# Kernel tuning notes

Hardware: AMD Instinct MI355X
Metric: run time of the kernel (lower is better)

Reference implementation:

```python
import jax, jax.numpy as jnp
import numpy as np

N, E, G = 50000, 800000, 512
D_NODE, D_EDGE, D_HID, D_OUT = 64, 16, 64, 1


def _lin(key, din, dout, bias=True):
    k1, k2 = jax.random.split(key)
    w = jax.random.normal(k1, (din, dout), jnp.float32) / np.sqrt(din)
    if bias:
        b = jax.random.normal(k2, (dout,), jnp.float32) * 0.01
        return w, b
    return w


def setup_inputs() -> dict:
    key = jax.random.key(0)
    ks = jax.random.split(key, 24)
    x = jax.random.normal(ks[0], (N, D_NODE), jnp.float32)
    edge_index = jax.random.randint(ks[1], (2, E), 0, N, jnp.int64)
    edge_attr = jax.random.normal(ks[2], (E, D_EDGE), jnp.float32)
    batch = jnp.sort(jax.random.randint(ks[3], (N,), 0, G, jnp.int64))
    wq1, bq1 = _lin(ks[4], D_NODE, D_HID)
    wk1, bk1 = _lin(ks[5], D_NODE, D_HID)
    wv1, bv1 = _lin(ks[6], D_NODE, D_HID)
    we1 = _lin(ks[7], D_EDGE, D_HID, bias=False)
    ws1, bs1 = _lin(ks[8], D_NODE, D_HID)
    wq2, bq2 = _lin(ks[9], D_HID, D_HID)
    wk2, bk2 = _lin(ks[10], D_HID, D_HID)
    wv2, bv2 = _lin(ks[11], D_HID, D_HID)
    we2 = _lin(ks[12], D_EDGE, D_HID, bias=False)
    ws2, bs2 = _lin(ks[13], D_HID, D_HID)
    w_fc1, b_fc1 = _lin(ks[14], D_HID, D_HID)
    w_fc2, b_fc2 = _lin(ks[15], D_HID, D_OUT)
    return dict(x=x, edge_index=edge_index, edge_attr=edge_attr, batch=batch,
                wq1=wq1, bq1=bq1, wk1=wk1, bk1=bk1, wv1=wv1, bv1=bv1, we1=we1, ws1=ws1, bs1=bs1,
                wq2=wq2, bq2=bq2, wk2=wk2, bk2=bk2, wv2=wv2, bv2=bv2, we2=we2, ws2=ws2, bs2=bs2,
                w_fc1=w_fc1, b_fc1=b_fc1, w_fc2=w_fc2, b_fc2=b_fc2)


def _leaky(z):
    return jnp.where(z >= 0, z, 0.01 * z)


def _transformer_conv(x, src, dst, e, wq, bq, wk, bk, wv, bv, we, ws, bs):
    # PyG TransformerConv, heads=1, concat=True, root_weight=True
    C = wq.shape[1]
    q = x @ wq + bq                      # [N,C]
    k = x @ wk + bk                      # [N,C]
    v = x @ wv + bv                      # [N,C]
    ee = e @ we                          # [E,C] (lin_edge, bias=False)
    ke = k[src] + ee                     # per-edge key
    ve = v[src] + ee                     # per-edge value
    score = jnp.sum(q[dst] * ke, axis=-1) / jnp.sqrt(jnp.float32(C))  # [E]
    m = jax.ops.segment_max(score, dst, num_segments=N)
    a = jnp.exp(score - m[dst])
    den = jax.ops.segment_sum(a, dst, num_segments=N)
    den = jnp.where(den == 0, 1.0, den)
    alpha = a / den[dst]
    agg = jax.ops.segment_sum(alpha[:, None] * ve, dst, num_segments=N)
    return agg + x @ ws + bs             # skip connection


def reference(x, edge_index, edge_attr, batch,
              wq1, bq1, wk1, bk1, wv1, bv1, we1, ws1, bs1,
              wq2, bq2, wk2, bk2, wv2, bv2, we2, ws2, bs2,
              w_fc1, b_fc1, w_fc2, b_fc2):
    src, dst = edge_index[0], edge_index[1]
    h = _leaky(_transformer_conv(x, src, dst, edge_attr, wq1, bq1, wk1, bk1, wv1, bv1, we1, ws1, bs1))
    atom_embs = _leaky(_transformer_conv(h, src, dst, edge_attr, wq2, bq2, wk2, bk2, wv2, bv2, we2, ws2, bs2))
    pooled = jax.ops.segment_sum(atom_embs, batch, num_segments=G)    # [G,C]
    norm = jnp.linalg.norm(pooled, axis=1, keepdims=True)
    h = pooled / jnp.maximum(norm, 1e-12)                             # F.normalize p=2
    h = _leaky(h @ w_fc1 + b_fc1)
    out = h @ w_fc2 + b_fc2
    return (out, atom_embs)
```

## Files before the change

kernel.cpp:

```cpp
#include <hip/hip_runtime.h>
#include <hip/hip_bf16.h>
#include <math.h>


typedef unsigned int uint32;
typedef unsigned short u16;

__device__ __forceinline__ uint32 f2bf(float x) {
    uint32 u = __float_as_uint(x);
    u += 0x7fffu + ((u >> 16) & 1u);
    return u >> 16;
}
__device__ __forceinline__ float bf2f(u16 h) {
    return __uint_as_float(((uint32)h) << 16);
}


__global__ void hist_kernel(const int* __restrict__ dst, int* __restrict__ deg, int E) {
    int e = blockIdx.x * blockDim.x + threadIdx.x;
    if (e < E) atomicAdd(&deg[dst[e]], 1);
}

__global__ void scan1_kernel(const int* __restrict__ deg, int* __restrict__ row_ptr,
                             int* __restrict__ totals, int N) {
    __shared__ int sh[1024];
    int tid = threadIdx.x;
    int i = blockIdx.x * 1024 + tid;
    int d = (i < N) ? deg[i] : 0;
    int val = d;
    sh[tid] = val;
    __syncthreads();
    for (int off = 1; off < 1024; off <<= 1) {
        int add = (tid >= off) ? sh[tid - off] : 0;
        __syncthreads();
        val += add;
        sh[tid] = val;
        __syncthreads();
    }
    if (i < N) row_ptr[i] = val - d;
    if (tid == 1023) totals[blockIdx.x] = val;
}

__global__ void scan2_kernel(int* totals, int nb) {
    int lane = threadIdx.x;
    int v = (lane < nb) ? totals[lane] : 0;
    #pragma unroll
    for (int off = 1; off < 64; off <<= 1) {
        int t = __shfl_up(v, off);
        if (lane >= off) v += t;
    }
    int ex = __shfl_up(v, 1);
    if (lane == 0) ex = 0;
    if (lane < nb) totals[lane] = ex;
}

__global__ void scan3_kernel(int* __restrict__ row_ptr, const int* __restrict__ totals,
                             int N, int E) {
    int i = blockIdx.x * blockDim.x + threadIdx.x;
    if (i < N) row_ptr[i] += totals[i >> 10];
    if (i == 0) row_ptr[N] = E;
}

__global__ void scatter_kernel(const int* __restrict__ dst, const int* __restrict__ row_ptr,
                               int* __restrict__ fill, int* __restrict__ csr_eid, int E) {
    int e = blockIdx.x * blockDim.x + threadIdx.x;
    if (e < E) {
        int d = dst[e];
        int pos = row_ptr[d] + atomicAdd(&fill[d], 1);
        csr_eid[pos] = e;
    }
}

__global__ void convert_kernel(const int* __restrict__ csr_eid, const int* __restrict__ src,
                               const float* __restrict__ ea,
                               int* __restrict__ csr_src, u16* __restrict__ ea16, int E) {
    int p = blockIdx.x * blockDim.x + threadIdx.x;
    if (p >= E) return;
    int e = csr_eid[p];
    csr_src[p] = src[e];
    const float4* ev = (const float4*)(ea + (size_t)e * 16);
    float4 q0 = ev[0], q1 = ev[1], q2 = ev[2], q3 = ev[3];
    uint32* o = (uint32*)(ea16 + (size_t)p * 16);
    o[0] = f2bf(q0.x) | (f2bf(q0.y) << 16);
    o[1] = f2bf(q0.z) | (f2bf(q0.w) << 16);
    o[2] = f2bf(q1.x) | (f2bf(q1.y) << 16);
    o[3] = f2bf(q1.z) | (f2bf(q1.w) << 16);
    o[4] = f2bf(q2.x) | (f2bf(q2.y) << 16);
    o[5] = f2bf(q2.z) | (f2bf(q2.w) << 16);
    o[6] = f2bf(q3.x) | (f2bf(q3.y) << 16);
    o[7] = f2bf(q3.z) | (f2bf(q3.w) << 16);
}


__global__ void wqe_kernel(const float* __restrict__ wq1, const float* __restrict__ bq1,
                           const float* __restrict__ we1,
                           const float* __restrict__ wq2, const float* __restrict__ bq2,
                           const float* __restrict__ we2,
                           float* __restrict__ A1, float* __restrict__ be1,
                           float* __restrict__ A2, float* __restrict__ be2) {
    const float* wq = blockIdx.x ? wq2 : wq1;
    const float* bq = blockIdx.x ? bq2 : bq1;
    const float* we = blockIdx.x ? we2 : we1;
    float* A  = blockIdx.x ? A2 : A1;
    float* be = blockIdx.x ? be2 : be1;
    int t = threadIdx.x;
    for (int idx = t; idx < 64 * 16; idx += 256) {
        int dd = idx >> 4, j = idx & 15;
        float acc = 0.f;
        for (int c = 0; c < 64; ++c) acc = fmaf(wq[dd * 64 + c], we[j * 64 + c], acc);
        A[idx] = acc * 0.125f;
    }
    if (t < 16) {
        float acc = 0.f;
        for (int c = 0; c < 64; ++c) acc = fmaf(bq[c], we[t * 64 + c], acc);
        be[t] = acc * 0.125f;
    }
}


__global__ __launch_bounds__(256) void qkvs_kernel(
    const float* __restrict__ xin,
    const float* __restrict__ wqm, const float* __restrict__ bqm,
    const float* __restrict__ wkm, const float* __restrict__ bkm,
    const float* __restrict__ wvm, const float* __restrict__ bvm,
    const float* __restrict__ wsm, const float* __restrict__ bsm,
    const float* __restrict__ Aq, const float* __restrict__ beq,
    float* __restrict__ qo, uint32* __restrict__ kvo,
    float* __restrict__ so, float* __restrict__ qeo, int N)
{
    int mtx = blockIdx.y;
    __shared__ float W0[64][64];
    __shared__ float W1[64][64];
    __shared__ float X[64][64];
    __shared__ float As[64][17];
    int t = threadIdx.x;
    int col = t & 63;
    int sub = t >> 6;

    const float* w0 = (mtx == 0) ? wqm : (mtx == 1) ? wkm : wsm;
    const float* b0p = (mtx == 0) ? bqm : (mtx == 1) ? bkm : bsm;
    for (int r = t; r < 1024; r += 256) ((float4*)W0)[r] = ((const float4*)w0)[r];
    if (mtx == 1)
        for (int r = t; r < 1024; r += 256) ((float4*)W1)[r] = ((const float4*)wvm)[r];
    if (mtx == 0)
        for (int r = t; r < 1024; r += 256) As[r >> 4][r & 15] = Aq[r];
    int n0 = blockIdx.x * 64;
    if (n0 + 64 <= N) {
        const float4* xi4 = (const float4*)(xin + (size_t)n0 * 64);
        for (int r = t; r < 1024; r += 256) ((float4*)X)[r] = xi4[r];
    } else {
        for (int r = t; r < 4096; r += 256) {
            int n = n0 + (r >> 6);
            X[r >> 6][r & 63] = (n < N) ? xin[(size_t)n * 64 + (r & 63)] : 0.f;
        }
    }
    __syncthreads();

    float b0 = b0p[col];
    float b1 = (mtx == 1) ? bvm[col] : 0.f;

    for (int nb = sub * 16; nb < sub * 16 + 16; nb += 8) {
        float a0[8], a1[8];
        #pragma unroll
        for (int u = 0; u < 8; ++u) { a0[u] = b0; a1[u] = b1; }
        if (mtx == 1) {
            for (int j = 0; j < 64; ++j) {
                float wk_ = W0[j][col], wv_ = W1[j][col];
                #pragma unroll
                for (int u = 0; u < 8; ++u) {
                    float xv = X[nb + u][j];
                    a0[u] = fmaf(xv, wk_, a0[u]);
                    a1[u] = fmaf(xv, wv_, a1[u]);
                }
            }
        } else {
            for (int j = 0; j < 64; ++j) {
                float wj = W0[j][col];
                #pragma unroll
                for (int u = 0; u < 8; ++u) a0[u] = fmaf(X[nb + u][j], wj, a0[u]);
            }
        }
        #pragma unroll
        for (int u = 0; u < 8; ++u) {
            int n = n0 + nb + u;
            if (n < N) {
                if (mtx == 0)      qo[(size_t)n * 64 + col] = a0[u] * 0.125f;
                else if (mtx == 2) so[(size_t)n * 64 + col] = a0[u];
                else kvo[(size_t)n * 64 + col] = f2bf(a0[u]) | (f2bf(a1[u]) << 16);
            }
        }
    }

    if (mtx == 0) {
        #pragma unroll
        for (int rep = 0; rep < 4; ++rep) {
            int idx = rep * 256 + t;
            int n = idx >> 4, j = idx & 15;
            float acc = beq[j];
            for (int c = 0; c < 64; ++c) acc = fmaf(X[n][c], As[c][j], acc);
            int gn = n0 + n;
            if (gn < N) qeo[(size_t)gn * 16 + j] = acc;
        }
    }
}


__global__ __launch_bounds__(256) void agg_kernel(
    const float* __restrict__ q, const uint32* __restrict__ kv,
    const float* __restrict__ qe, const float* __restrict__ we,
    const u16* __restrict__ ea16,
    const int* __restrict__ row_ptr, const int* __restrict__ csr_src,
    const float* __restrict__ skip_in, float* __restrict__ hout,
    const int* __restrict__ batch, float* __restrict__ pooled, int N)
{
    int lane = threadIdx.x & 63;
    int wid = (blockIdx.x << 2) + (threadIdx.x >> 6);
    if (wid >= N) return;
    int i = __builtin_amdgcn_readfirstlane(wid);

    int grp = lane >> 4;
    int pos = lane & 15;

    float4 qv = ((const float4*)(q + (size_t)i * 64))[pos];
    float qel = qe[(size_t)i * 16 + pos];
    float wer[16];
    #pragma unroll
    for (int j = 0; j < 16; ++j) wer[j] = we[j * 64 + lane];

    float den = 0.f, aj = 0.f;
    float o4x = 0.f, o4y = 0.f, o4z = 0.f, o4w = 0.f;

    int beg = row_ptr[i], end = row_ptr[i + 1];
    int last = end - 1;
    for (int p = beg; p < end; p += 8) {
        int egA = p + grp, egB = p + 4 + grp;
        int siA = (egA < end) ? egA : last;
        int siB = (egB < end) ? egB : last;
        int sA = csr_src[siA], sB = csr_src[siB];
        uint4 kbA = ((const uint4*)(kv + (size_t)sA * 64))[pos];
        uint4 kbB = ((const uint4*)(kv + (size_t)sB * 64))[pos];
        float eaA = bf2f(ea16[(size_t)p * 16 + lane]);
        float eaB = bf2f(ea16[(size_t)(p + 4) * 16 + lane]);

        float pa = eaA * qel, pb = eaB * qel;
        pa = fmaf(qv.x, __uint_as_float(kbA.x << 16), pa);
        pb = fmaf(qv.x, __uint_as_float(kbB.x << 16), pb);
        pa = fmaf(qv.y, __uint_as_float(kbA.y << 16), pa);
        pb = fmaf(qv.y, __uint_as_float(kbB.y << 16), pb);
        pa = fmaf(qv.z, __uint_as_float(kbA.z << 16), pa);
        pb = fmaf(qv.z, __uint_as_float(kbB.z << 16), pb);
        pa = fmaf(qv.w, __uint_as_float(kbA.w << 16), pa);
        pb = fmaf(qv.w, __uint_as_float(kbB.w << 16), pb);
        pa += __shfl_xor(pa, 1);  pb += __shfl_xor(pb, 1);
        pa += __shfl_xor(pa, 2);  pb += __shfl_xor(pb, 2);
        pa += __shfl_xor(pa, 4);  pb += __shfl_xor(pb, 4);
        pa += __shfl_xor(pa, 8);  pb += __shfl_xor(pb, 8);
        float scA = (egA < end) ? pa : -1e30f;
        float scB = (egB < end) ? pb : -1e30f;
        float wA = __expf(scA), wB = __expf(scB);

        den += wA + wB;
        aj = fmaf(wA, eaA, aj);
        aj = fmaf(wB, eaB, aj);
        o4x = fmaf(wA, __uint_as_float(kbA.x & 0xffff0000u), o4x);
        o4y = fmaf(wA, __uint_as_float(kbA.y & 0xffff0000u), o4y);
        o4z = fmaf(wA, __uint_as_float(kbA.z & 0xffff0000u), o4z);
        o4w = fmaf(wA, __uint_as_float(kbA.w & 0xffff0000u), o4w);
        o4x = fmaf(wB, __uint_as_float(kbB.x & 0xffff0000u), o4x);
        o4y = fmaf(wB, __uint_as_float(kbB.y & 0xffff0000u), o4y);
        o4z = fmaf(wB, __uint_as_float(kbB.z & 0xffff0000u), o4z);
        o4w = fmaf(wB, __uint_as_float(kbB.w & 0xffff0000u), o4w);
    }

    o4x += __shfl_xor(o4x, 16); o4x += __shfl_xor(o4x, 32);
    o4y += __shfl_xor(o4y, 16); o4y += __shfl_xor(o4y, 32);
    o4z += __shfl_xor(o4z, 16); o4z += __shfl_xor(o4z, 32);
    o4w += __shfl_xor(o4w, 16); o4w += __shfl_xor(o4w, 32);
    aj  += __shfl_xor(aj, 16);  aj  += __shfl_xor(aj, 32);
    den += __shfl_xor(den, 16); den += __shfl_xor(den, 32);

    int srcl = lane >> 2;
    float t0 = __shfl(o4x, srcl), t1 = __shfl(o4y, srcl);
    float t2 = __shfl(o4z, srcl), t3 = __shfl(o4w, srcl);
    int r2 = lane & 3;
    float o = (r2 == 0) ? t0 : (r2 == 1) ? t1 : (r2 == 2) ? t2 : t3;

    #pragma unroll
    for (int j = 0; j < 16; ++j) o = fmaf(__shfl(aj, j), wer[j], o);

    float dinv = (den > 0.f) ? 1.f / den : 0.f;
    float r = fmaf(o, dinv, skip_in[(size_t)i * 64 + lane]);
    r = (r >= 0.f) ? r : 0.01f * r;
    hout[(size_t)i * 64 + lane] = r;
    if (pooled) atomicAdd(&pooled[(size_t)batch[i] * 64 + lane], r);
}


__global__ void head_kernel(const float* __restrict__ pooled,
                            const float* __restrict__ w1, const float* __restrict__ b1,
                            const float* __restrict__ w2, const float* __restrict__ b2,
                            float* __restrict__ out, int G) {
    int g = blockIdx.x;
    int lane = threadIdx.x;
    __shared__ float hl[64];
    float p = pooled[g * 64 + lane];
    float ss = p * p;
    #pragma unroll
    for (int off = 32; off; off >>= 1) ss += __shfl_xor(ss, off);
    float hn = p / fmaxf(sqrtf(ss), 1e-12f);
    hl[lane] = hn;
    __syncthreads();
    float acc = b1[lane];
    #pragma unroll
    for (int j = 0; j < 64; ++j) acc = fmaf(hl[j], w1[j * 64 + lane], acc);
    acc = (acc >= 0.f) ? acc : 0.01f * acc;
    float r = acc * w2[lane];
    #pragma unroll
    for (int off = 32; off; off >>= 1) r += __shfl_xor(r, off);
    if (lane == 0) out[g] = r + b2[0];
}


extern "C" void kernel_launch(void* const* d_in, const int* in_sizes, int n_in,
                              void* d_out, int out_size, void* d_ws, size_t ws_size,
                              hipStream_t stream) {
    const float* x     = (const float*)d_in[0];
    const int*   ei    = (const int*)  d_in[1];
    const float* ea    = (const float*)d_in[2];
    const int*   batch = (const int*)  d_in[3];
    const float *wq1=(const float*)d_in[4],  *bq1=(const float*)d_in[5];
    const float *wk1=(const float*)d_in[6],  *bk1=(const float*)d_in[7];
    const float *wv1=(const float*)d_in[8],  *bv1=(const float*)d_in[9];
    const float *we1=(const float*)d_in[10];
    const float *ws1=(const float*)d_in[11], *bs1=(const float*)d_in[12];
    const float *wq2=(const float*)d_in[13], *bq2=(const float*)d_in[14];
    const float *wk2=(const float*)d_in[15], *bk2=(const float*)d_in[16];
    const float *wv2=(const float*)d_in[17], *bv2=(const float*)d_in[18];
    const float *we2=(const float*)d_in[19];
    const float *ws2=(const float*)d_in[20], *bs2=(const float*)d_in[21];
    const float *wf1=(const float*)d_in[22], *bf1=(const float*)d_in[23];
    const float *wf2=(const float*)d_in[24], *bf2=(const float*)d_in[25];

    int N = in_sizes[0] / 64;
    int E = in_sizes[2] / 16;
    int G = out_size - N * 64;

    const int* srcA = ei;
    const int* dstA = ei + E;

    char* w = (char*)d_ws;
    float*  qb      = (float*)w;  w += (size_t)N * 64 * 4;
    uint32* kvb     = (uint32*)w; w += (size_t)N * 64 * 4;
    float*  hb      = (float*)w;  w += (size_t)N * 64 * 4;
    float*  qeb     = (float*)w;  w += (size_t)N * 16 * 4;
    float*  pooled  = (float*)w;  w += (size_t)G * 64 * 4;
    int* row_ptr    = (int*)w;    w += (size_t)(N + 1) * 4;
    int* totals     = (int*)w;    w += 256 * 4;
    float* A1       = (float*)w;  w += 1024 * 4;
    float* be1      = (float*)w;  w += 16 * 4;
    float* A2       = (float*)w;  w += 1024 * 4;
    float* be2      = (float*)w;  w += 16 * 4;
    int* csr_src    = (int*)w;    w += (size_t)E * 4;
    int* csr_eid    = (int*)w;    w += (size_t)E * 4;
    u16* ea16       = (u16*)w;    w += (size_t)(E * 16 + 128) * 2;
    int* deg  = (int*)qb;
    int* fill = (int*)qb + N;

    hipMemsetAsync(deg, 0, (size_t)2 * N * 4, stream);
    hipMemsetAsync(pooled, 0, (size_t)G * 64 * 4, stream);

    const int TB = 256;
    wqe_kernel<<<2, 256, 0, stream>>>(wq1, bq1, we1, wq2, bq2, we2, A1, be1, A2, be2);
    hist_kernel<<<(E + TB - 1) / TB, TB, 0, stream>>>(dstA, deg, E);
    int nb = (N + 1023) / 1024;
    scan1_kernel<<<nb, 1024, 0, stream>>>(deg, row_ptr, totals, N);
    scan2_kernel<<<1, 64, 0, stream>>>(totals, nb);
    scan3_kernel<<<(N + TB - 1) / TB, TB, 0, stream>>>(row_ptr, totals, N, E);
    scatter_kernel<<<(E + TB - 1) / TB, TB, 0, stream>>>(dstA, row_ptr, fill, csr_eid, E);
    convert_kernel<<<(E + TB - 1) / TB, TB, 0, stream>>>(csr_eid, srcA, ea,
                                                         csr_src, ea16, E);

    float* outp = (float*)d_out;
    float* atom = outp + G;

    dim3 qgrid((N + 63) / 64, 3);
    int aggBlocks = (N + 3) / 4;

    qkvs_kernel<<<qgrid, 256, 0, stream>>>(x, wq1, bq1, wk1, bk1, wv1, bv1, ws1, bs1,
                                           A1, be1, qb, kvb, hb, qeb, N);
    agg_kernel<<<aggBlocks, 256, 0, stream>>>(qb, kvb, qeb, we1, ea16, row_ptr, csr_src,
                                              hb, hb, nullptr, nullptr, N);

    qkvs_kernel<<<qgrid, 256, 0, stream>>>(hb, wq2, bq2, wk2, bk2, wv2, bv2, ws2, bs2,
                                           A2, be2, qb, kvb, atom, qeb, N);
    agg_kernel<<<aggBlocks, 256, 0, stream>>>(qb, kvb, qeb, we2, ea16, row_ptr, csr_src,
                                              atom, atom, batch, pooled, N);

    head_kernel<<<G, 64, 0, stream>>>(pooled, wf1, bf1, wf2, bf2, outp, G);
}
```

Baseline: 449.4 us.

## Compute node projections with bf16 MFMA and pre-transposed packed weights

Replaces the scalar FP32 shared-memory GEMM for the Q/K/V/skip and Q·We projections with bf16 MFMA 16x16x32 instructions. A prep kernel transposes and packs all layer weights to bf16, including the folded query-edge matrix. One launch per layer now computes every projection, where the old version used three grid slices that each reloaded X. This lowers FP32 ALU work and redundant input reads, but rounds inputs and weights to bf16, which reduces the precision of q, skip and qe.

```diff
diff --git a/kernel.cpp b/kernel.cpp
--- a/kernel.cpp
+++ b/kernel.cpp
@@ -5,6 +5,8 @@
 
 typedef unsigned int uint32;
 typedef unsigned short u16;
+typedef __attribute__((ext_vector_type(8))) short short8;
+typedef __attribute__((ext_vector_type(4))) float f32x4;
 
 __device__ __forceinline__ uint32 f2bf(float x) {
     uint32 u = __float_as_uint(x);
@@ -92,23 +94,38 @@
 }
 
 
-__global__ void wqe_kernel(const float* __restrict__ wq1, const float* __restrict__ bq1,
-                           const float* __restrict__ we1,
-                           const float* __restrict__ wq2, const float* __restrict__ bq2,
-                           const float* __restrict__ we2,
-                           float* __restrict__ A1, float* __restrict__ be1,
-                           float* __restrict__ A2, float* __restrict__ be2) {
-    const float* wq = blockIdx.x ? wq2 : wq1;
-    const float* bq = blockIdx.x ? bq2 : bq1;
-    const float* we = blockIdx.x ? we2 : we1;
-    float* A  = blockIdx.x ? A2 : A1;
-    float* be = blockIdx.x ? be2 : be1;
+__global__ void wprep_kernel(
+    const float* __restrict__ wq1, const float* __restrict__ bq1,
+    const float* __restrict__ wk1, const float* __restrict__ wv1,
+    const float* __restrict__ ws1, const float* __restrict__ we1,
+    const float* __restrict__ wq2, const float* __restrict__ bq2,
+    const float* __restrict__ wk2, const float* __restrict__ wv2,
+    const float* __restrict__ ws2, const float* __restrict__ we2,
+    u16* __restrict__ wt1, float* __restrict__ be1,
+    u16* __restrict__ wt2, float* __restrict__ be2)
+{
+    int L = blockIdx.x;
+    const float* wq = L ? wq2 : wq1;
+    const float* bq = L ? bq2 : bq1;
+    const float* wk = L ? wk2 : wk1;
+    const float* wv = L ? wv2 : wv1;
+    const float* ws = L ? ws2 : ws1;
+    const float* we = L ? we2 : we1;
+    u16* wt = L ? wt2 : wt1;
+    float* be = L ? be2 : be1;
     int t = threadIdx.x;
-    for (int idx = t; idx < 64 * 16; idx += 256) {
-        int dd = idx >> 4, j = idx & 15;
+    for (int i = t; i < 4096; i += 256) {
+        int k = i >> 6, n = i & 63;
+        wt[0 * 4096 + n * 64 + k] = (u16)f2bf(wq[k * 64 + n]);
+        wt[1 * 4096 + n * 64 + k] = (u16)f2bf(wk[k * 64 + n]);
+        wt[2 * 4096 + n * 64 + k] = (u16)f2bf(wv[k * 64 + n]);
+        wt[3 * 4096 + n * 64 + k] = (u16)f2bf(ws[k * 64 + n]);
+    }
+    for (int i = t; i < 1024; i += 256) {
+        int j = i >> 6, k = i & 63;
         float acc = 0.f;
-        for (int c = 0; c < 64; ++c) acc = fmaf(wq[dd * 64 + c], we[j * 64 + c], acc);
-        A[idx] = acc * 0.125f;
+        for (int c = 0; c < 64; ++c) acc = fmaf(wq[k * 64 + c], we[j * 64 + c], acc);
+        wt[4 * 4096 + j * 64 + k] = (u16)f2bf(acc * 0.125f);
     }
     if (t < 16) {
         float acc = 0.f;
@@ -118,89 +135,82 @@
 }
 
 
-__global__ __launch_bounds__(256) void qkvs_kernel(
-    const float* __restrict__ xin,
-    const float* __restrict__ wqm, const float* __restrict__ bqm,
-    const float* __restrict__ wkm, const float* __restrict__ bkm,
-    const float* __restrict__ wvm, const float* __restrict__ bvm,
-    const float* __restrict__ wsm, const float* __restrict__ bsm,
-    const float* __restrict__ Aq, const float* __restrict__ beq,
+__global__ __launch_bounds__(256) void qkvs_mfma(
+    const float* __restrict__ xin, const u16* __restrict__ wt,
+    const float* __restrict__ bq, const float* __restrict__ bk,
+    const float* __restrict__ bv, const float* __restrict__ bs,
+    const float* __restrict__ be,
     float* __restrict__ qo, uint32* __restrict__ kvo,
     float* __restrict__ so, float* __restrict__ qeo, int N)
 {
-    int mtx = blockIdx.y;
-    __shared__ float W0[64][64];
-    __shared__ float W1[64][64];
-    __shared__ float X[64][64];
-    __shared__ float As[64][17];
-    int t = threadIdx.x;
-    int col = t & 63;
-    int sub = t >> 6;
-
-    const float* w0 = (mtx == 0) ? wqm : (mtx == 1) ? wkm : wsm;
-    const float* b0p = (mtx == 0) ? bqm : (mtx == 1) ? bkm : bsm;
-    for (int r = t; r < 1024; r += 256) ((float4*)W0)[r] = ((const float4*)w0)[r];
-    if (mtx == 1)
-        for (int r = t; r < 1024; r += 256) ((float4*)W1)[r] = ((const float4*)wvm)[r];
-    if (mtx == 0)
-        for (int r = t; r < 1024; r += 256) As[r >> 4][r & 15] = Aq[r];
-    int n0 = blockIdx.x * 64;
-    if (n0 + 64 <= N) {
-        const float4* xi4 = (const float4*)(xin + (size_t)n0 * 64);
-        for (int r = t; r < 1024; r += 256) ((float4*)X)[r] = xi4[r];
-    } else {
-        for (int r = t; r < 4096; r += 256) {
-            int n = n0 + (r >> 6);
-            X[r >> 6][r & 63] = (n < N) ? xin[(size_t)n * 64 + (r & 63)] : 0.f;
+    int wave = threadIdx.x >> 6;
+    int lane = threadIdx.x & 63;
+    int quad = lane >> 4;
+    int l16 = lane & 15;
+    int n0 = blockIdx.x * 64 + wave * 16;
+    int row = n0 + l16;
+    int rn = (row < N) ? row : (N - 1);
+
+    const float4* xr = (const float4*)(xin + (size_t)rn * 64);
+    float4 u0 = xr[quad * 2 + 0], u1 = xr[quad * 2 + 1];
+    float4 u2 = xr[8 + quad * 2 + 0], u3 = xr[8 + quad * 2 + 1];
+    short8 a0, a1;
+    a0[0] = (short)f2bf(u0.x); a0[1] = (short)f2bf(u0.y);
+    a0[2] = (short)f2bf(u0.z); a0[3] = (short)f2bf(u0.w);
+    a0[4] = (short)f2bf(u1.x); a0[5] = (short)f2bf(u1.y);
+    a0[6] = (short)f2bf(u1.z); a0[7] = (short)f2bf(u1.w);
+    a1[0] = (short)f2bf(u2.x); a1[1] = (short)f2bf(u2.y);
+    a1[2] = (short)f2bf(u2.z); a1[3] = (short)f2bf(u2.w);
+    a1[4] = (short)f2bf(u3.x); a1[5] = (short)f2bf(u3.y);
+    a1[6] = (short)f2bf(u3.z); a1[7] = (short)f2bf(u3.w);
+
+    const short8* w8 = (const short8*)wt;
+
+    f32x4 acc[4][4];
+    #pragma unroll
+    for (int m = 0; m < 4; ++m)
+        #pragma unroll
+        for (int c = 0; c < 4; ++c) acc[m][c] = (f32x4){0.f, 0.f, 0.f, 0.f};
+    f32x4 aqe = (f32x4){0.f, 0.f, 0.f, 0.f};
+
+    #pragma unroll
+    for (int m = 0; m < 4; ++m) {
+        #pragma unroll
+        for (int c = 0; c < 4; ++c) {
+            short8 b0 = w8[m * 512 + (c * 16 + l16) * 8 + quad];
+            short8 b1 = w8[m * 512 + (c * 16 + l16) * 8 + 4 + quad];
+            acc[m][c] = __builtin_amdgcn_mfma_f32_16x16x32_bf16(a0, b0, acc[m][c], 0, 0, 0);
+            acc[m][c] = __builtin_amdgcn_mfma_f32_16x16x32_bf16(a1, b1, acc[m][c], 0, 0, 0);
         }
     }
-    __syncthreads();
-
-    float b0 = b0p[col];
-    float b1 = (mtx == 1) ? bvm[col] : 0.f;
-
-    for (int nb = sub * 16; nb < sub * 16 + 16; nb += 8) {
-        float a0[8], a1[8];
+    {
+        short8 b0 = w8[4 * 512 + l16 * 8 + quad];
+        short8 b1 = w8[4 * 512 + l16 * 8 + 4 + quad];
+        aqe = __builtin_amdgcn_mfma_f32_16x16x32_bf16(a0, b0, aqe, 0, 0, 0);
+        aqe = __builtin_amdgcn_mfma_f32_16x16x32_bf16(a1, b1, aqe, 0, 0, 0);
+    }
+
+    int node0 = n0 + quad * 4;
+    #pragma unroll
+    for (int c = 0; c < 4; ++c) {
+        int col = c * 16 + l16;
+        float bQ = bq[col], bK = bk[col], bV = bv[col], bS = bs[col];
         #pragma unroll
-        for (int u = 0; u < 8; ++u) { a0[u] = b0; a1[u] = b1; }
-        if (mtx == 1) {
-            for (int j = 0; j < 64; ++j) {
-                float wk_ = W0[j][col], wv_ = W1[j][col];
-                #pragma unroll
-                for (int u = 0; u < 8; ++u) {
-                    float xv = X[nb + u][j];
-                    a0[u] = fmaf(xv, wk_, a0[u]);
-                    a1[u] = fmaf(xv, wv_, a1[u]);
-                }
-            }
-        } else {
-            for (int j = 0; j < 64; ++j) {
-                float wj = W0[j][col];
-                #pragma unroll
-                for (int u = 0; u < 8; ++u) a0[u] = fmaf(X[nb + u][j], wj, a0[u]);
+        for (int r = 0; r < 4; ++r) {
+            int node = node0 + r;
+            if (node < N) {
+                size_t off = (size_t)node * 64 + col;
+                qo[off] = (acc[0][c][r] + bQ) * 0.125f;
+                kvo[off] = f2bf(acc[1][c][r] + bK) | (f2bf(acc[2][c][r] + bV) << 16);
+                so[off] = acc[3][c][r] + bS;
             }
         }
-        #pragma unroll
-        for (int u = 0; u < 8; ++u) {
-            int n = n0 + nb + u;
-            if (n < N) {
-                if (mtx == 0)      qo[(size_t)n * 64 + col] = a0[u] * 0.125f;
-                else if (mtx == 2) so[(size_t)n * 64 + col] = a0[u];
-                else kvo[(size_t)n * 64 + col] = f2bf(a0[u]) | (f2bf(a1[u]) << 16);
-            }
-        }
-    }
-
-    if (mtx == 0) {
-        #pragma unroll
-        for (int rep = 0; rep < 4; ++rep) {
-            int idx = rep * 256 + t;
-            int n = idx >> 4, j = idx & 15;
-            float acc = beq[j];
-            for (int c = 0; c < 64; ++c) acc = fmaf(X[n][c], As[c][j], acc);
-            int gn = n0 + n;
-            if (gn < N) qeo[(size_t)gn * 16 + j] = acc;
-        }
+    }
+    float beL = be[l16];
+    #pragma unroll
+    for (int r = 0; r < 4; ++r) {
+        int node = node0 + r;
+        if (node < N) qeo[(size_t)node * 16 + l16] = aqe[r] + beL;
     }
 }
 
@@ -356,9 +366,9 @@
     float*  pooled  = (float*)w;  w += (size_t)G * 64 * 4;
     int* row_ptr    = (int*)w;    w += (size_t)(N + 1) * 4;
     int* totals     = (int*)w;    w += 256 * 4;
-    float* A1       = (float*)w;  w += 1024 * 4;
+    u16* wt1        = (u16*)w;    w += (4 * 4096 + 1024) * 2;
+    u16* wt2        = (u16*)w;    w += (4 * 4096 + 1024) * 2;
     float* be1      = (float*)w;  w += 16 * 4;
-    float* A2       = (float*)w;  w += 1024 * 4;
     float* be2      = (float*)w;  w += 16 * 4;
     int* csr_src    = (int*)w;    w += (size_t)E * 4;
     int* csr_eid    = (int*)w;    w += (size_t)E * 4;
@@ -370,7 +380,9 @@
     hipMemsetAsync(pooled, 0, (size_t)G * 64 * 4, stream);
 
     const int TB = 256;
-    wqe_kernel<<<2, 256, 0, stream>>>(wq1, bq1, we1, wq2, bq2, we2, A1, be1, A2, be2);
+    wprep_kernel<<<2, 256, 0, stream>>>(wq1, bq1, wk1, wv1, ws1, we1,
+                                        wq2, bq2, wk2, wv2, ws2, we2,
+                                        wt1, be1, wt2, be2);
     hist_kernel<<<(E + TB - 1) / TB, TB, 0, stream>>>(dstA, deg, E);
     int nb = (N + 1023) / 1024;
     scan1_kernel<<<nb, 1024, 0, stream>>>(deg, row_ptr, totals, N);
@@ -383,16 +395,16 @@
     float* outp = (float*)d_out;
     float* atom = outp + G;
 
-    dim3 qgrid((N + 63) / 64, 3);
+    int qBlocks = (N + 63) / 64;
     int aggBlocks = (N + 3) / 4;
 
-    qkvs_kernel<<<qgrid, 256, 0, stream>>>(x, wq1, bq1, wk1, bk1, wv1, bv1, ws1, bs1,
-                                           A1, be1, qb, kvb, hb, qeb, N);
+    qkvs_mfma<<<qBlocks, 256, 0, stream>>>(x, wt1, bq1, bk1, bv1, bs1, be1,
+                                           qb, kvb, hb, qeb, N);
     agg_kernel<<<aggBlocks, 256, 0, stream>>>(qb, kvb, qeb, we1, ea16, row_ptr, csr_src,
                                               hb, hb, nullptr, nullptr, N);
 
-    qkvs_kernel<<<qgrid, 256, 0, stream>>>(hb, wq2, bq2, wk2, bk2, wv2, bv2, ws2, bs2,
-                                           A2, be2, qb, kvb, atom, qeb, N);
+    qkvs_mfma<<<qBlocks, 256, 0, stream>>>(hb, wt2, bq2, bk2, bv2, bs2, be2,
+                                           qb, kvb, atom, qeb, N);
     agg_kernel<<<aggBlocks, 256, 0, stream>>>(qb, kvb, qeb, we2, ea16, row_ptr, csr_src,
                                               atom, atom, batch, pooled, N);
 
```

Result: faster. 415.3 us (-7.6%).
